# Kernel tuning notes

Measured on AMD Instinct MI355X. Metric: run time of the kernel, lower is better.

Reference implementation:

```python
import jax, jax.numpy as jnp
import numpy as np

DIM = 48
D_STATE = 16
D_CONV = 4
EXPAND = 2
D_INNER = DIM * EXPAND          # 96
DT_RANK = (DIM + 15) // 16      # 3
EPS = 1e-5


def _interp2x_align_corners(x, axis):
    """Linear 2x upsample along one axis with align_corners=True."""
    n = x.shape[axis]
    out = 2 * n
    pos = jnp.arange(out, dtype=jnp.float32) * (n - 1) / (out - 1)
    lo = jnp.floor(pos).astype(jnp.int32)
    hi = jnp.minimum(lo + 1, n - 1)
    w = (pos - lo.astype(jnp.float32)).astype(x.dtype)
    shape = [1] * x.ndim
    shape[axis] = out
    w = w.reshape(shape)
    return jnp.take(x, lo, axis=axis) * (1 - w) + jnp.take(x, hi, axis=axis) * w


def _upsample_trilinear2x(x):
    for axis in (2, 3, 4):
        x = _interp2x_align_corners(x, axis)
    return x


def _conv3d(x, w, b, pad):
    y = jax.lax.conv_general_dilated(
        x, w, window_strides=(1, 1, 1), padding=[(pad, pad)] * 3,
        dimension_numbers=('NCDHW', 'OIDHW', 'NCDHW'))
    return y + b[None, :, None, None, None]


def _instance_norm(x):
    m = x.mean(axis=(2, 3, 4), keepdims=True)
    v = x.var(axis=(2, 3, 4), keepdims=True)  # biased var, as PyTorch InstanceNorm3d
    return (x - m) / jnp.sqrt(v + EPS)


def _mamba(u, in_proj_w, conv1d_w, conv1d_b, x_proj_w, dt_proj_w, dt_proj_b,
           A_log, D_param, out_proj_w):
    # u: (B, L, d_model)
    Bsz, L, _ = u.shape
    xz = jnp.einsum('bld,ed->ble', u, in_proj_w)        # (B, L, 2*Di)
    xi, z = jnp.split(xz, 2, axis=-1)                   # each (B, L, Di)
    # depthwise causal conv1d (pad left d_conv-1, crop to L == mamba's slice)
    xpad = jnp.pad(xi.transpose(0, 2, 1), ((0, 0), (0, 0), (D_CONV - 1, 0)))
    xc = jax.lax.conv_general_dilated(
        xpad, conv1d_w, window_strides=(1,), padding=[(0, 0)],
        dimension_numbers=('NCH', 'OIH', 'NCH'), feature_group_count=D_INNER)
    xs = jax.nn.silu((xc + conv1d_b[None, :, None]).transpose(0, 2, 1))  # (B, L, Di)

    dbc = jnp.einsum('bld,ed->ble', xs, x_proj_w)       # (B, L, dt_rank+2*N)
    dt, Bm, Cm = jnp.split(dbc, [DT_RANK, DT_RANK + D_STATE], axis=-1)
    delta = jax.nn.softplus(jnp.einsum('blr,dr->bld', dt, dt_proj_w) + dt_proj_b)

    A = -jnp.exp(A_log)                                  # (Di, N)
    dA = jnp.exp(jnp.einsum('bld,dn->bldn', delta, A))   # (B, L, Di, N)
    dBx = jnp.einsum('bld,bln->bldn', delta * xs, Bm)    # (B, L, Di, N)

    def step(h, inp):
        dA_t, dBx_t, C_t = inp                           # (B,Di,N),(B,Di,N),(B,N)
        h = dA_t * h + dBx_t
        y = jnp.einsum('bdn,bn->bd', h, C_t)
        return h, y

    h0 = jnp.zeros((Bsz, D_INNER, D_STATE), xs.dtype)
    _, ys = jax.lax.scan(step, h0,
                         (dA.transpose(1, 0, 2, 3), dBx.transpose(1, 0, 2, 3),
                          Cm.transpose(1, 0, 2)))
    y = ys.transpose(1, 0, 2) + D_param[None, None, :] * xs
    y = y * jax.nn.silu(z)
    return jnp.einsum('bld,ed->ble', y, out_proj_w)      # (B, L, d_model)


def setup_inputs() -> dict:
    key = jax.random.key(0)
    ks = jax.random.split(key, 16)
    s = 0.05
    f32 = jnp.float32
    inp = {
        'x': jax.random.normal(ks[0], (2, DIM, 12, 12, 12), f32),
        'Hx': jax.random.normal(ks[1], (2, DIM * 2, 24, 24, 24), f32),
        'W1': jax.random.normal(ks[2], (DIM, DIM * 3, 1, 1, 1), f32) * s,
        'b1': jax.random.normal(ks[3], (DIM,), f32) * s,
        'W2': jax.random.normal(ks[4], (DIM, DIM, 3, 3, 3), f32) * s,
        'b2': jax.random.normal(ks[5], (DIM,), f32) * s,
        'W3': jax.random.normal(ks[6], (DIM, DIM, 1, 1, 1), f32) * s,
        'b3': jax.random.normal(ks[7], (DIM,), f32) * s,
        'in_proj_w': jax.random.normal(ks[8], (2 * D_INNER, DIM), f32) * s,
        'conv1d_w': jax.random.normal(ks[9], (D_INNER, 1, D_CONV), f32) * s,
        'conv1d_b': jax.random.normal(ks[10], (D_INNER,), f32) * s,
        'x_proj_w': jax.random.normal(ks[11], (DT_RANK + 2 * D_STATE, D_INNER), f32) * s,
        'dt_proj_w': jax.random.normal(ks[12], (D_INNER, DT_RANK), f32) * s,
        'dt_proj_b': jax.random.normal(ks[13], (D_INNER,), f32) * 0.1,
        'A_log': jnp.log(jnp.tile(jnp.arange(1, D_STATE + 1, dtype=f32)[None, :],
                                  (D_INNER, 1))),
        'D_param': jnp.ones((D_INNER,), f32),
        'out_proj_w': jax.random.normal(ks[14], (DIM, D_INNER), f32) * s,
    }
    return inp


def reference(x, Hx, W1, b1, W2, b2, W3, b3, in_proj_w, conv1d_w, conv1d_b,
              x_proj_w, dt_proj_w, dt_proj_b, A_log, D_param, out_proj_w):
    up = _upsample_trilinear2x(x)                         # (B, dim, 2H, 2W, 2T)
    h = jnp.concatenate([up, Hx], axis=1)                 # (B, 3*dim, ...)
    h = _conv3d(h, W1, b1, 0)
    h = _conv3d(h, W2, b2, 1)
    h = _conv3d(h, W3, b3, 0)
    Lx = jax.nn.selu(_instance_norm(h))
    B, C, H, W, T = Lx.shape
    u = Lx.reshape(B, C, H * W * T).transpose(0, 2, 1)    # (B, L, C)
    ym = _mamba(u, in_proj_w, conv1d_w, conv1d_b, x_proj_w, dt_proj_w,
                dt_proj_b, A_log, D_param, out_proj_w)
    out = ym.transpose(0, 2, 1).reshape(B, C, H, W, T) + Lx
    return out
```

## Files before the change

### kernel.cpp

```cpp
#include <hip/hip_runtime.h>
#include <math.h>

#define NB 2
#define NCH 48
#define P 13824
#define DI 96
#define NSTATE 16
#define L 13824
#define CHUNK 128
#define NCK 108
#define TL 64

__device__ __forceinline__ float siluf(float x) { return x / (1.f + __expf(-x)); }
__device__ __forceinline__ float softplusf(float x) {
    return x > 0.f ? x + log1pf(expf(-x)) : log1pf(expf(x));
}

__global__ __launch_bounds__(256) void k_wtrans(const float* __restrict__ W2,
    const float* __restrict__ W1, const float* __restrict__ W3,
    const float* __restrict__ Wop, float* __restrict__ Wt, float* __restrict__ W1t,
    float* __restrict__ W3t, float* __restrict__ Wopt)
{
    int i = blockIdx.x * 256 + threadIdx.x;
    if (i < 62208) {
        int o = i / (48 * 27); int r = i % (48 * 27); int c = r / 27; int tap = r % 27;
        int og = o / 12, oi = o % 12;
        Wt[(((og * 48 + c) * 27 + tap) * 12) + oi] = W2[i];
    } else if (i < 62208 + 6912) {
        int j = i - 62208; int o = j / 144, c = j % 144;
        W1t[c * 48 + o] = W1[j];
    } else if (i < 62208 + 6912 + 2304) {
        int j = i - 62208 - 6912; int o = j / 48, c = j % 48;
        W3t[c * 48 + o] = W3[j];
    } else if (i < 62208 + 6912 + 2304 + 4608) {
        int j = i - 62208 - 6912 - 2304; int o = j / 96, q = j % 96;
        Wopt[q * 48 + o] = Wop[j];
    }
}

__global__ __launch_bounds__(128) void k_conv1(const float* __restrict__ x,
    const float* __restrict__ Hx, const float* __restrict__ W1t,
    const float* __restrict__ b1, float* __restrict__ h1)
{
    int t = blockIdx.x * 128 + threadIdx.x;
    int oh = blockIdx.y * 24;
    int b = t / P, p = t % P;
    int zi = p / 576, yi = (p / 24) % 24, xi_ = p % 24;
    float fpos; int z0, z1, y0, y1, x0, x1; float wz, wy, wx;
    fpos = (float)(zi * 11) / 23.0f; z0 = (int)floorf(fpos); wz = fpos - z0; z1 = min(z0 + 1, 11);
    fpos = (float)(yi * 11) / 23.0f; y0 = (int)floorf(fpos); wy = fpos - y0; y1 = min(y0 + 1, 11);
    fpos = (float)(xi_ * 11) / 23.0f; x0 = (int)floorf(fpos); wx = fpos - x0; x1 = min(x0 + 1, 11);
    int o000 = (z0*12+y0)*12+x0, o001 = (z0*12+y0)*12+x1;
    int o010 = (z0*12+y1)*12+x0, o011 = (z0*12+y1)*12+x1;
    int o100 = (z1*12+y0)*12+x0, o101 = (z1*12+y0)*12+x1;
    int o110 = (z1*12+y1)*12+x0, o111 = (z1*12+y1)*12+x1;
    float uz = 1.f - wz, uy = 1.f - wy, ux = 1.f - wx;
    float w000 = uz*uy*ux, w001 = uz*uy*wx, w010 = uz*wy*ux, w011 = uz*wy*wx;
    float w100 = wz*uy*ux, w101 = wz*uy*wx, w110 = wz*wy*ux, w111 = wz*wy*wx;

    float acc[24];
#pragma unroll
    for (int o = 0; o < 24; ++o) acc[o] = b1[oh + o];
    const float* xb = x + (size_t)b * 48 * 1728;
    for (int c0 = 0; c0 < 48; c0 += 4) {
        float a[4][8];
#pragma unroll
        for (int j = 0; j < 4; ++j) {
            const float* xc = xb + (c0 + j) * 1728;
            a[j][0] = xc[o000]; a[j][1] = xc[o001]; a[j][2] = xc[o010]; a[j][3] = xc[o011];
            a[j][4] = xc[o100]; a[j][5] = xc[o101]; a[j][6] = xc[o110]; a[j][7] = xc[o111];
        }
#pragma unroll
        for (int j = 0; j < 4; ++j) {
            float v = a[j][0]*w000 + a[j][1]*w001 + a[j][2]*w010 + a[j][3]*w011
                    + a[j][4]*w100 + a[j][5]*w101 + a[j][6]*w110 + a[j][7]*w111;
            const float* wr = W1t + (c0 + j) * 48 + oh;
#pragma unroll
            for (int o = 0; o < 24; ++o) acc[o] = fmaf(wr[o], v, acc[o]);
        }
    }
    const float* hb = Hx + (size_t)b * 96 * P + p;
    for (int c0 = 0; c0 < 96; c0 += 8) {
        float v[8];
#pragma unroll
        for (int j = 0; j < 8; ++j) v[j] = hb[(size_t)(c0 + j) * P];
#pragma unroll
        for (int j = 0; j < 8; ++j) {
            const float* wr = W1t + (48 + c0 + j) * 48 + oh;
#pragma unroll
            for (int o = 0; o < 24; ++o) acc[o] = fmaf(wr[o], v[j], acc[o]);
        }
    }
    float* out = h1 + (size_t)b * 48 * P + p;
#pragma unroll
    for (int o = 0; o < 24; ++o) out[(size_t)(oh+o) * P] = acc[o];
}

__global__ __launch_bounds__(512) void k_conv2(const float* __restrict__ h1,
    const float* __restrict__ Wt, const float* __restrict__ b2, float* __restrict__ h2)
{
    __shared__ float tile[48 * 240];
    int blk = blockIdx.x;
    int b = blk / 216; int r = blk % 216;
    int tz = r / 36, ty = (r / 6) % 6, tx = r % 6;
    int z0 = tz*4 - 1, y0 = ty*4 - 1, x0 = tx*4 - 1;
    for (int i = threadIdx.x; i < 48 * 216; i += 512) {
        int c = i / 216; int q = i % 216;
        int lz = q / 36, ly = (q / 6) % 6, lx = q % 6;
        int gz = z0 + lz, gy = y0 + ly, gx = x0 + lx;
        float v = 0.f;
        if ((unsigned)gz < 24u && (unsigned)gy < 24u && (unsigned)gx < 24u)
            v = h1[((size_t)(b*48 + c)) * P + (gz*24 + gy)*24 + gx];
        tile[c*240 + lz*40 + ly*6 + lx] = v;
    }
    __syncthreads();
    int lp = threadIdx.x & 63;
    int w  = __builtin_amdgcn_readfirstlane((int)(threadIdx.x >> 6));
    int og = w & 3, cc = w >> 2;
    int lz = lp >> 4, ly = (lp >> 2) & 3, lx = lp & 3;
    float acc[12];
#pragma unroll
    for (int i = 0; i < 12; ++i) acc[i] = cc ? 0.f : b2[og*12 + i];
    const float* wb = Wt + ((size_t)og * 48 + cc * 24) * 27 * 12;
    const float* tb = tile + cc * 24 * 240;
    for (int cl = 0; cl < 24; ++cl) {
        const float* tc = tb + cl * 240;
        const float* wc = wb + cl * 27 * 12;
#pragma unroll
        for (int dz = 0; dz < 3; ++dz)
#pragma unroll
        for (int dy = 0; dy < 3; ++dy)
#pragma unroll
        for (int dx = 0; dx < 3; ++dx) {
            float v = tc[(lz+dz)*40 + (ly+dy)*6 + (lx+dx)];
            const float* wt = wc + ((dz*3 + dy)*3 + dx) * 12;
#pragma unroll
            for (int i = 0; i < 12; ++i)
                acc[i] = fmaf(wt[i], v, acc[i]);
        }
    }
    __syncthreads();
    if (cc == 1) {
        float* ex = tile + og * 768;
#pragma unroll
        for (int i = 0; i < 12; ++i) ex[i*64 + lp] = acc[i];
    }
    __syncthreads();
    if (cc == 0) {
        const float* ex = tile + og * 768;
        int gz = tz*4 + lz, gy = ty*4 + ly, gx = tx*4 + lx;
        size_t pp = (size_t)(gz*24 + gy)*24 + gx;
#pragma unroll
        for (int i = 0; i < 12; ++i)
            h2[((size_t)(b*48) + og*12 + i) * P + pp] = acc[i] + ex[i*64 + lp];
    }
}

__global__ __launch_bounds__(128) void k_conv3(const float* __restrict__ h2,
    const float* __restrict__ W3t, const float* __restrict__ b3, float* __restrict__ h3)
{
    int t = blockIdx.x * 128 + threadIdx.x;
    int oh = blockIdx.y * 24;
    int b = t / P, p = t % P;
    float acc[24];
#pragma unroll
    for (int o = 0; o < 24; ++o) acc[o] = b3[oh + o];
    const float* hb = h2 + (size_t)b * 48 * P + p;
    for (int c0 = 0; c0 < 48; c0 += 8) {
        float v[8];
#pragma unroll
        for (int j = 0; j < 8; ++j) v[j] = hb[(size_t)(c0 + j) * P];
#pragma unroll
        for (int j = 0; j < 8; ++j) {
            const float* wr = W3t + (c0 + j) * 48 + oh;
#pragma unroll
            for (int o = 0; o < 24; ++o) acc[o] = fmaf(wr[o], v[j], acc[o]);
        }
    }
    float* out = h3 + (size_t)b * 48 * P + p;
#pragma unroll
    for (int o = 0; o < 24; ++o) out[(size_t)(oh+o) * P] = acc[o];
}

__global__ __launch_bounds__(256) void k_in_stats(const float* __restrict__ h3,
                                                  float* __restrict__ stats)
{
    int bc = blockIdx.x;
    const float4* src4 = (const float4*)(h3 + (size_t)bc * P);
    float s = 0.f, s2 = 0.f;
    for (int i = threadIdx.x; i < 3456; i += 256) {
        float4 v = src4[i];
        s  += v.x + v.y + v.z + v.w;
        s2 += v.x*v.x + v.y*v.y + v.z*v.z + v.w*v.w;
    }
    __shared__ float rs[4], rs2[4];
    for (int off = 32; off; off >>= 1) { s += __shfl_down(s, off); s2 += __shfl_down(s2, off); }
    int wid = threadIdx.x >> 6;
    if ((threadIdx.x & 63) == 0) { rs[wid] = s; rs2[wid] = s2; }
    __syncthreads();
    if (threadIdx.x == 0) {
        s = rs[0] + rs[1] + rs[2] + rs[3];
        s2 = rs2[0] + rs2[1] + rs2[2] + rs2[3];
        float m = s / (float)P;
        float var = s2 / (float)P - m * m;
        stats[bc*2] = m;
        stats[bc*2 + 1] = rsqrtf(var + 1e-5f);
    }
}

__global__ __launch_bounds__(256) void k_in_apply(float* __restrict__ h3,
                                                  const float* __restrict__ stats)
{
    int t = blockIdx.x * 256 + threadIdx.x;
    int bc = t / P;
    float m = stats[bc*2], istd = stats[bc*2 + 1];
    float v = (h3[t] - m) * istd;
    const float kScale = 1.0507009873554805f, kAlpha = 1.6732632423543772f;
    h3[t] = v > 0.f ? kScale * v : kScale * kAlpha * expm1f(v);
}

__global__ __launch_bounds__(192) void k_inproj(const float* __restrict__ Lx,
    const float* __restrict__ Wip, float* __restrict__ xi, float* __restrict__ z)
{
    __shared__ float u[48 * 32];
    int b = blockIdx.x / 432; int l0 = (blockIdx.x % 432) * 32;
    for (int i = threadIdx.x; i < 48 * 32; i += 192) {
        int c = i >> 5, ll = i & 31;
        u[i] = Lx[((size_t)(b*48) + c) * P + l0 + ll];
    }
    __syncthreads();
    int e = threadIdx.x;
    float w[48];
#pragma unroll
    for (int c = 0; c < 48; ++c) w[c] = Wip[e*48 + c];
    float* dst = (e < 96) ? (xi + ((size_t)b * L + l0) * 96 + e)
                          : (z  + ((size_t)b * L + l0) * 96 + (e - 96));
    for (int ll = 0; ll < 32; ++ll) {
        float acc = 0.f;
#pragma unroll
        for (int c = 0; c < 48; ++c) acc = fmaf(w[c], u[c*32 + ll], acc);
        dst[(size_t)ll * 96] = acc;
    }
}

__global__ __launch_bounds__(256) void k_fxproj(const float* __restrict__ xi,
    const float* __restrict__ cw, const float* __restrict__ cb,
    const float* __restrict__ Wxp, const float* __restrict__ Wdt,
    const float* __restrict__ bdt, float* __restrict__ xs,
    float* __restrict__ delta, float* __restrict__ Bm, float* __restrict__ Cm)
{
    __shared__ float xs_t[TL][100];
    __shared__ float wx_t[35][100];
    __shared__ float wd_t[96][4];
    __shared__ float dt_t[TL][4];
    int blk = blockIdx.x;
    int b = blk / 216; int l0 = (blk % 216) * TL;
    int tid = threadIdx.x;

    for (int i = tid; i < 35 * 96; i += 256) wx_t[i / 96][i % 96] = Wxp[i];
    for (int i = tid; i < 96 * 3; i += 256) wd_t[i / 3][i % 3] = Wdt[i];
    for (int i = tid; i < 96; i += 256) wd_t[i][3] = bdt[i];

    int row = tid >> 2;
    int d0 = (tid & 3) * 24;
    int l = l0 + row;
    size_t t_glob = (size_t)b * L + l;
    const float* xib = xi + (size_t)b * L * 96;
    float* xsg = xs + t_glob * 96 + d0;
    int ls0 = l - 3;
#pragma unroll
    for (int jq = 0; jq < 6; ++jq) {
        int d = d0 + jq * 4;
        float4 t0 = *(const float4*)(cw + 4 * (d + 0));
        float4 t1 = *(const float4*)(cw + 4 * (d + 1));
        float4 t2 = *(const float4*)(cw + 4 * (d + 2));
        float4 t3 = *(const float4*)(cw + 4 * (d + 3));
        float4 acc = *(const float4*)(cb + d);
        float4 q0 = {0.f,0.f,0.f,0.f}, q1 = q0, q2 = q0;
        if (ls0 + 0 >= 0) q0 = *(const float4*)(xib + (size_t)(ls0 + 0) * 96 + d);
        if (ls0 + 1 >= 0) q1 = *(const float4*)(xib + (size_t)(ls0 + 1) * 96 + d);
        if (ls0 + 2 >= 0) q2 = *(const float4*)(xib + (size_t)(ls0 + 2) * 96 + d);
        float4 q3 = *(const float4*)(xib + (size_t)(ls0 + 3) * 96 + d);
        acc.x += t0.x*q0.x + t0.y*q1.x + t0.z*q2.x + t0.w*q3.x;
        acc.y += t1.x*q0.y + t1.y*q1.y + t1.z*q2.y + t1.w*q3.y;
        acc.z += t2.x*q0.z + t2.y*q1.z + t2.z*q2.z + t2.w*q3.z;
        acc.w += t3.x*q0.w + t3.y*q1.w + t3.z*q2.w + t3.w*q3.w;
        acc.x = siluf(acc.x); acc.y = siluf(acc.y);
        acc.z = siluf(acc.z); acc.w = siluf(acc.w);
        *(float4*)(&xs_t[row][d0 + jq * 4]) = acc;
        *(float4*)(xsg + jq * 4) = acc;
    }
    __syncthreads();

    int cq = tid & 3;
    float acc9[9];
#pragma unroll
    for (int k = 0; k < 9; ++k) acc9[k] = 0.f;
    const float* xrow = &xs_t[row][0];
#pragma unroll 4
    for (int j = 0; j < 24; ++j) {
        float4 xv = *(const float4*)(xrow + 4 * j);
#pragma unroll
        for (int k = 0; k < 9; ++k) {
            if (k < 8 || cq < 3) {
                int e = cq + 4 * k;
                float4 wv = *(const float4*)(&wx_t[e][4 * j]);
                acc9[k] = fmaf(wv.x, xv.x, fmaf(wv.y, xv.y,
                          fmaf(wv.z, xv.z, fmaf(wv.w, xv.w, acc9[k]))));
            }
        }
    }
#pragma unroll
    for (int k = 0; k < 9; ++k) {
        if (k < 8 || cq < 3) {
            int e = cq + 4 * k;
            if (e < 3)       dt_t[row][e] = acc9[k];
            else if (e < 19) Bm[t_glob * 16 + (e - 3)]  = acc9[k];
            else             Cm[t_glob * 16 + (e - 19)] = acc9[k];
        }
    }
    __syncthreads();

    float dt0 = dt_t[row][0], dt1 = dt_t[row][1], dt2 = dt_t[row][2];
    float* dl = delta + t_glob * 96 + d0;
#pragma unroll
    for (int jq = 0; jq < 6; ++jq) {
        float4 o;
        {
            float4 wv = *(const float4*)(&wd_t[d0 + jq*4 + 0][0]);
            o.x = softplusf(fmaf(wv.x, dt0, fmaf(wv.y, dt1, fmaf(wv.z, dt2, wv.w))));
        }
        {
            float4 wv = *(const float4*)(&wd_t[d0 + jq*4 + 1][0]);
            o.y = softplusf(fmaf(wv.x, dt0, fmaf(wv.y, dt1, fmaf(wv.z, dt2, wv.w))));
        }
        {
            float4 wv = *(const float4*)(&wd_t[d0 + jq*4 + 2][0]);
            o.z = softplusf(fmaf(wv.x, dt0, fmaf(wv.y, dt1, fmaf(wv.z, dt2, wv.w))));
        }
        {
            float4 wv = *(const float4*)(&wd_t[d0 + jq*4 + 3][0]);
            o.w = softplusf(fmaf(wv.x, dt0, fmaf(wv.y, dt1, fmaf(wv.z, dt2, wv.w))));
        }
        *(float4*)(dl + jq * 4) = o;
    }
}

__global__ __launch_bounds__(256) void k_scan1(const float* __restrict__ delta,
    const float* __restrict__ xs, const float* __restrict__ Bm,
    const float* __restrict__ Alog, float* __restrict__ Aprod, float* __restrict__ hend)
{
    int wid = (blockIdx.x * 256 + threadIdx.x) >> 6;
    int lane = threadIdx.x & 63;
    int dg = wid % 24; int ch = (wid / 24) % NCK; int b = wid / (24 * NCK);
    int dl = lane >> 4, n = lane & 15;
    int d = dg * 4 + dl;
    float A = -__expf(Alog[d*16 + n]);
    float h = 0.f, ap = 1.f;
    int t0 = ch * CHUNK;
    const float* dp = delta + ((size_t)b * L + t0) * 96 + d;
    const float* xp = xs    + ((size_t)b * L + t0) * 96 + d;
    const float* bp = Bm    + ((size_t)b * L + t0) * 16 + n;

    float dA0, dA1, dA2, dA3, xA0, xA1, xA2, xA3, bA0, bA1, bA2, bA3;
    float dB0, dB1, dB2, dB3, xB0, xB1, xB2, xB3, bB0, bB1, bB2, bB3;
#define LD1(s, T) do { \
    d##s##0 = dp[(size_t)(T)*96];     x##s##0 = xp[(size_t)(T)*96];     b##s##0 = bp[(size_t)(T)*16]; \
    d##s##1 = dp[(size_t)((T)+1)*96]; x##s##1 = xp[(size_t)((T)+1)*96]; b##s##1 = bp[(size_t)((T)+1)*16]; \
    d##s##2 = dp[(size_t)((T)+2)*96]; x##s##2 = xp[(size_t)((T)+2)*96]; b##s##2 = bp[(size_t)((T)+2)*16]; \
    d##s##3 = dp[(size_t)((T)+3)*96]; x##s##3 = xp[(size_t)((T)+3)*96]; b##s##3 = bp[(size_t)((T)+3)*16]; \
  } while (0)
#define CMP1(s) do { \
    float e0 = __expf(d##s##0 * A); float e1 = __expf(d##s##1 * A); \
    float e2 = __expf(d##s##2 * A); float e3 = __expf(d##s##3 * A); \
    h = fmaf(e0, h, d##s##0 * x##s##0 * b##s##0); \
    h = fmaf(e1, h, d##s##1 * x##s##1 * b##s##1); \
    h = fmaf(e2, h, d##s##2 * x##s##2 * b##s##2); \
    h = fmaf(e3, h, d##s##3 * x##s##3 * b##s##3); \
    ap *= e0 * e1 * e2 * e3; \
  } while (0)

    LD1(A, 0);
#pragma unroll 1
    for (int t = 0; t < CHUNK; t += 8) {
        LD1(B, t + 4);
        CMP1(A);
        if (t + 8 < CHUNK) LD1(A, t + 8);
        CMP1(B);
    }
#undef LD1
#undef CMP1
    size_t idx = (((size_t)b * NCK + ch) * 96 + d) * 16 + n;
    Aprod[idx] = ap;
    hend[idx]  = h;
}

__global__ __launch_bounds__(256) void k_scan2(const float* __restrict__ Aprod,
    const float* __restrict__ hend, float* __restrict__ hin)
{
    int t = blockIdx.x * 256 + threadIdx.x;
    int b = t / 1536; int dn = t % 1536;
    const float* ap = Aprod + (size_t)b * NCK * 1536 + dn;
    const float* he = hend  + (size_t)b * NCK * 1536 + dn;
    float* hi       = hin   + (size_t)b * NCK * 1536 + dn;
    float carry = 0.f;
    float aA0, aA1, aA2, aA3, hA0, hA1, hA2, hA3;
    float aB0, aB1, aB2, aB3, hB0, hB1, hB2, hB3;
#define LD2(s, J) do { \
    a##s##0 = ap[(size_t)(J)*1536];     h##s##0 = he[(size_t)(J)*1536]; \
    a##s##1 = ap[(size_t)((J)+1)*1536]; h##s##1 = he[(size_t)((J)+1)*1536]; \
    a##s##2 = ap[(size_t)((J)+2)*1536]; h##s##2 = he[(size_t)((J)+2)*1536]; \
    a##s##3 = ap[(size_t)((J)+3)*1536]; h##s##3 = he[(size_t)((J)+3)*1536]; \
  } while (0)
#define CMP2(s, J) do { \
    hi[(size_t)(J)*1536]     = carry; carry = fmaf(a##s##0, carry, h##s##0); \
    hi[(size_t)((J)+1)*1536] = carry; carry = fmaf(a##s##1, carry, h##s##1); \
    hi[(size_t)((J)+2)*1536] = carry; carry = fmaf(a##s##2, carry, h##s##2); \
    hi[(size_t)((J)+3)*1536] = carry; carry = fmaf(a##s##3, carry, h##s##3); \
  } while (0)
    LD2(A, 0);
#pragma unroll 1
    for (int j = 0; j < 104; j += 8) {
        LD2(B, j + 4);
        CMP2(A, j);
        if (j + 8 < NCK) LD2(A, j + 8);
        CMP2(B, j + 4);
    }
    LD2(A, 104);
    CMP2(A, 104);
#undef LD2
#undef CMP2
}

__global__ __launch_bounds__(256) void k_scan3(const float* __restrict__ delta,
    float* __restrict__ xs, const float* __restrict__ Bm, const float* __restrict__ Cm,
    const float* __restrict__ z, const float* __restrict__ Alog,
    const float* __restrict__ Dp, const float* __restrict__ hin)
{
    int wid = (blockIdx.x * 256 + threadIdx.x) >> 6;
    int lane = threadIdx.x & 63;
    int dg = wid % 24; int ch = (wid / 24) % NCK; int b = wid / (24 * NCK);
    int dl = lane >> 4, n = lane & 15;
    int d = dg * 4 + dl;
    float A = -__expf(Alog[d*16 + n]);
    float Dv = Dp[d];
    size_t cidx = (((size_t)b * NCK + ch) * 96 + d) * 16 + n;
    float h = hin[cidx];
    int t0 = ch * CHUNK;
    const float* dp = delta + ((size_t)b * L + t0) * 96 + d;
    float* xp       = xs    + ((size_t)b * L + t0) * 96 + d;
    const float* bp = Bm    + ((size_t)b * L + t0) * 16 + n;
    const float* cp = Cm    + ((size_t)b * L + t0) * 16 + n;
    const float* zp = z     + ((size_t)b * L + t0) * 96 + d;

    float dA0, dA1, dA2, dA3, xA0, xA1, xA2, xA3, bA0, bA1, bA2, bA3, cA0, cA1, cA2, cA3, zA0, zA1, zA2, zA3;
    float dB0, dB1, dB2, dB3, xB0, xB1, xB2, xB3, bB0, bB1, bB2, bB3, cB0, cB1, cB2, cB3, zB0, zB1, zB2, zB3;
#define LD3(s, T) do { \
    d##s##0 = dp[(size_t)(T)*96];     x##s##0 = xp[(size_t)(T)*96];     b##s##0 = bp[(size_t)(T)*16]; \
    c##s##0 = cp[(size_t)(T)*16];     z##s##0 = zp[(size_t)(T)*96]; \
    d##s##1 = dp[(size_t)((T)+1)*96]; x##s##1 = xp[(size_t)((T)+1)*96]; b##s##1 = bp[(size_t)((T)+1)*16]; \
    c##s##1 = cp[(size_t)((T)+1)*16]; z##s##1 = zp[(size_t)((T)+1)*96]; \
    d##s##2 = dp[(size_t)((T)+2)*96]; x##s##2 = xp[(size_t)((T)+2)*96]; b##s##2 = bp[(size_t)((T)+2)*16]; \
    c##s##2 = cp[(size_t)((T)+2)*16]; z##s##2 = zp[(size_t)((T)+2)*96]; \
    d##s##3 = dp[(size_t)((T)+3)*96]; x##s##3 = xp[(size_t)((T)+3)*96]; b##s##3 = bp[(size_t)((T)+3)*16]; \
    c##s##3 = cp[(size_t)((T)+3)*16]; z##s##3 = zp[(size_t)((T)+3)*96]; \
  } while (0)
#define STEP3(DEL, XV, BV, CV, ZV, T) do { \
    float dAv = __expf((DEL) * A); \
    h = fmaf(dAv, h, (DEL) * (XV) * (BV)); \
    float yc = h * (CV); \
    yc += __shfl_xor(yc, 8); \
    yc += __shfl_xor(yc, 4); \
    yc += __shfl_xor(yc, 2); \
    yc += __shfl_xor(yc, 1); \
    if (n == 0) xp[(size_t)(T)*96] = fmaf(Dv, (XV), yc) * siluf(ZV); \
  } while (0)
#define CMP3(s, T) do { \
    STEP3(d##s##0, x##s##0, b##s##0, c##s##0, z##s##0, (T)); \
    STEP3(d##s##1, x##s##1, b##s##1, c##s##1, z##s##1, (T)+1); \
    STEP3(d##s##2, x##s##2, b##s##2, c##s##2, z##s##2, (T)+2); \
    STEP3(d##s##3, x##s##3, b##s##3, c##s##3, z##s##3, (T)+3); \
  } while (0)

    LD3(A, 0);
#pragma unroll 1
    for (int t = 0; t < CHUNK; t += 8) {
        LD3(B, t + 4);
        CMP3(A, t);
        if (t + 8 < CHUNK) LD3(A, t + 8);
        CMP3(B, t + 4);
    }
#undef LD3
#undef STEP3
#undef CMP3
}

__global__ __launch_bounds__(128) void k_outproj(const float* __restrict__ y,
    const float* __restrict__ Wopt, const float* __restrict__ Lx, float* __restrict__ out)
{
    int t = blockIdx.x * 128 + threadIdx.x;
    int oh = blockIdx.y * 24;
    int b = t / P, p = t % P;
    const float* yr = y + (size_t)t * 96;
    float acc[24];
#pragma unroll
    for (int o = 0; o < 24; ++o) acc[o] = 0.f;
#pragma unroll
    for (int i = 0; i < 24; ++i) {
        float4 v4 = ((const float4*)yr)[i];
        const float* w0 = Wopt + (i*4) * 48 + oh;
        const float* w1 = Wopt + (i*4 + 1) * 48 + oh;
        const float* w2 = Wopt + (i*4 + 2) * 48 + oh;
        const float* w3 = Wopt + (i*4 + 3) * 48 + oh;
#pragma unroll
        for (int o = 0; o < 24; ++o) {
            acc[o] = fmaf(w0[o], v4.x, acc[o]);
            acc[o] = fmaf(w1[o], v4.y, acc[o]);
            acc[o] = fmaf(w2[o], v4.z, acc[o]);
            acc[o] = fmaf(w3[o], v4.w, acc[o]);
        }
    }
    const float* lx = Lx + (size_t)b * 48 * P + p;
    float* op = out + (size_t)b * 48 * P + p;
#pragma unroll
    for (int o = 0; o < 24; ++o) op[(size_t)(oh+o) * P] = acc[o] + lx[(size_t)(oh+o) * P];
}

extern "C" void kernel_launch(void* const* d_in, const int* in_sizes, int n_in,
                              void* d_out, int out_size, void* d_ws, size_t ws_size,
                              hipStream_t stream) {
    const float* x        = (const float*)d_in[0];
    const float* Hx       = (const float*)d_in[1];
    const float* W1       = (const float*)d_in[2];
    const float* b1       = (const float*)d_in[3];
    const float* W2       = (const float*)d_in[4];
    const float* b2       = (const float*)d_in[5];
    const float* W3       = (const float*)d_in[6];
    const float* b3       = (const float*)d_in[7];
    const float* in_proj  = (const float*)d_in[8];
    const float* conv1d_w = (const float*)d_in[9];
    const float* conv1d_b = (const float*)d_in[10];
    const float* x_proj   = (const float*)d_in[11];
    const float* dt_proj  = (const float*)d_in[12];
    const float* dt_bias  = (const float*)d_in[13];
    const float* A_log    = (const float*)d_in[14];
    const float* D_param  = (const float*)d_in[15];
    const float* out_proj = (const float*)d_in[16];
    float* out = (float*)d_out;

    float* ws = (float*)d_ws;
    const size_t SZ_BCP = (size_t)NB * 48 * P;
    const size_t SZ_BLD = (size_t)NB * L * 96;
    const size_t SZ_BLN = (size_t)NB * L * 16;
    const size_t SZ_CK  = (size_t)NB * NCK * 1536;
    float* bufA  = ws;
    float* bufB  = bufA + SZ_BCP;
    float* bufC  = bufB + SZ_BCP;
    float* xib   = bufC + SZ_BCP;
    float* zb    = xib  + SZ_BLD;
    float* xsb   = zb   + SZ_BLD;
    float* Bmb   = xsb  + SZ_BLD;
    float* Cmb   = Bmb  + SZ_BLN;
    float* Apr   = Cmb  + SZ_BLN;
    float* hendb = Apr  + SZ_CK;
    float* hinb  = hendb+ SZ_CK;
    float* stats = hinb + SZ_CK;
    float* Wtb   = stats + 192;
    float* W1tb  = Wtb + 62208;
    float* W3tb  = W1tb + 6912;
    float* Woptb = W3tb + 2304;
    float* deltab = bufA;

    k_wtrans<<<297, 256, 0, stream>>>(W2, W1, W3, out_proj, Wtb, W1tb, W3tb, Woptb);
    k_conv1<<<dim3(216, 2), 128, 0, stream>>>(x, Hx, W1tb, b1, bufA);
    k_conv2<<<NB * 216, 512, 0, stream>>>(bufA, Wtb, b2, bufB);
    k_conv3<<<dim3(216, 2), 128, 0, stream>>>(bufB, W3tb, b3, bufC);
    k_in_stats<<<NB * 48, 256, 0, stream>>>(bufC, stats);
    k_in_apply<<<5184, 256, 0, stream>>>(bufC, stats);
    k_inproj<<<NB * 432, 192, 0, stream>>>(bufC, in_proj, xib, zb);
    k_fxproj<<<NB * 216, 256, 0, stream>>>(xib, conv1d_w, conv1d_b, x_proj, dt_proj,
                                           dt_bias, xsb, deltab, Bmb, Cmb);
    k_scan1<<<(NB * NCK * 24) / 4, 256, 0, stream>>>(deltab, xsb, Bmb, A_log, Apr, hendb);
    k_scan2<<<12, 256, 0, stream>>>(Apr, hendb, hinb);
    k_scan3<<<(NB * NCK * 24) / 4, 256, 0, stream>>>(deltab, xsb, Bmb, Cmb, zb, A_log,
                                                     D_param, hinb);
    k_outproj<<<dim3(216, 2), 128, 0, stream>>>(xsb, Woptb, bufC, out);
}
```

Measured before the change: 286.8 us.

## Fuse conv2 with 1x1 conv3, merge instance-norm passes, drop inproj LDS staging

The 1x1x1 conv3 now runs inside the conv2 kernel. Conv2 results are staged in shared memory and each wave computes 6 output channels, so the h2 round trip through global memory and one launch are gone. Instance-norm statistics and the normalize+SELU apply become a single kernel per channel that rereads its slice, which removes a launch and the stats buffer. In-proj now reads Lx directly from global memory with register accumulators instead of staging it in LDS. The trade-offs are serialized per-channel work in the norm kernel (only 96 blocks) and higher register pressure in in-proj.

```diff
diff --git a/kernel.cpp b/kernel.cpp
--- a/kernel.cpp
+++ b/kernel.cpp
@@ -96,8 +96,10 @@
     for (int o = 0; o < 24; ++o) out[(size_t)(oh+o) * P] = acc[o];
 }
 
-__global__ __launch_bounds__(512) void k_conv2(const float* __restrict__ h1,
-    const float* __restrict__ Wt, const float* __restrict__ b2, float* __restrict__ h2)
+__global__ __launch_bounds__(512) void k_conv23(const float* __restrict__ h1,
+    const float* __restrict__ Wt, const float* __restrict__ b2,
+    const float* __restrict__ W3t, const float* __restrict__ b3,
+    float* __restrict__ h3)
 {
     __shared__ float tile[48 * 240];
     int blk = blockIdx.x;
@@ -148,52 +150,41 @@
     __syncthreads();
     if (cc == 0) {
         const float* ex = tile + og * 768;
-        int gz = tz*4 + lz, gy = ty*4 + ly, gx = tx*4 + lx;
-        size_t pp = (size_t)(gz*24 + gy)*24 + gx;
+        float* ht = tile + 3072;
 #pragma unroll
         for (int i = 0; i < 12; ++i)
-            h2[((size_t)(b*48) + og*12 + i) * P + pp] = acc[i] + ex[i*64 + lp];
-    }
-}
-
-__global__ __launch_bounds__(128) void k_conv3(const float* __restrict__ h2,
-    const float* __restrict__ W3t, const float* __restrict__ b3, float* __restrict__ h3)
-{
-    int t = blockIdx.x * 128 + threadIdx.x;
-    int oh = blockIdx.y * 24;
-    int b = t / P, p = t % P;
-    float acc[24];
-#pragma unroll
-    for (int o = 0; o < 24; ++o) acc[o] = b3[oh + o];
-    const float* hb = h2 + (size_t)b * 48 * P + p;
-    for (int c0 = 0; c0 < 48; c0 += 8) {
-        float v[8];
-#pragma unroll
-        for (int j = 0; j < 8; ++j) v[j] = hb[(size_t)(c0 + j) * P];
-#pragma unroll
-        for (int j = 0; j < 8; ++j) {
-            const float* wr = W3t + (c0 + j) * 48 + oh;
-#pragma unroll
-            for (int o = 0; o < 24; ++o) acc[o] = fmaf(wr[o], v[j], acc[o]);
-        }
-    }
-    float* out = h3 + (size_t)b * 48 * P + p;
-#pragma unroll
-    for (int o = 0; o < 24; ++o) out[(size_t)(oh+o) * P] = acc[o];
-}
-
-__global__ __launch_bounds__(256) void k_in_stats(const float* __restrict__ h3,
-                                                  float* __restrict__ stats)
+            ht[(og*12 + i)*64 + lp] = acc[i] + ex[i*64 + lp];
+    }
+    __syncthreads();
+    const float* ht = tile + 3072;
+    int oc0 = w * 6;
+    float acc3[6];
+#pragma unroll
+    for (int j = 0; j < 6; ++j) acc3[j] = b3[oc0 + j];
+    for (int c = 0; c < 48; ++c) {
+        float v = ht[c*64 + lp];
+        const float* wr = W3t + c*48 + oc0;
+#pragma unroll
+        for (int j = 0; j < 6; ++j) acc3[j] = fmaf(wr[j], v, acc3[j]);
+    }
+    int gz = tz*4 + lz, gy = ty*4 + ly, gx = tx*4 + lx;
+    size_t pp = (size_t)(gz*24 + gy)*24 + gx;
+#pragma unroll
+    for (int j = 0; j < 6; ++j)
+        h3[((size_t)(b*48) + oc0 + j) * P + pp] = acc3[j];
+}
+
+__global__ __launch_bounds__(256) void k_instnorm(float* __restrict__ h3)
 {
     int bc = blockIdx.x;
-    const float4* src4 = (const float4*)(h3 + (size_t)bc * P);
+    float4* src = (float4*)(h3 + (size_t)bc * P);
     float s = 0.f, s2 = 0.f;
     for (int i = threadIdx.x; i < 3456; i += 256) {
-        float4 v = src4[i];
+        float4 v = src[i];
         s  += v.x + v.y + v.z + v.w;
         s2 += v.x*v.x + v.y*v.y + v.z*v.z + v.w*v.w;
     }
-    __shared__ float rs[4], rs2[4];
+    __shared__ float rs[4], rs2[4], mv[2];
     for (int off = 32; off; off >>= 1) { s += __shfl_down(s, off); s2 += __shfl_down(s2, off); }
     int wid = threadIdx.x >> 6;
     if ((threadIdx.x & 63) == 0) { rs[wid] = s; rs2[wid] = s2; }
@@ -203,44 +194,45 @@
         s2 = rs2[0] + rs2[1] + rs2[2] + rs2[3];
         float m = s / (float)P;
         float var = s2 / (float)P - m * m;
-        stats[bc*2] = m;
-        stats[bc*2 + 1] = rsqrtf(var + 1e-5f);
-    }
-}
-
-__global__ __launch_bounds__(256) void k_in_apply(float* __restrict__ h3,
-                                                  const float* __restrict__ stats)
-{
-    int t = blockIdx.x * 256 + threadIdx.x;
-    int bc = t / P;
-    float m = stats[bc*2], istd = stats[bc*2 + 1];
-    float v = (h3[t] - m) * istd;
-    const float kScale = 1.0507009873554805f, kAlpha = 1.6732632423543772f;
-    h3[t] = v > 0.f ? kScale * v : kScale * kAlpha * expm1f(v);
+        mv[0] = m; mv[1] = rsqrtf(var + 1e-5f);
+    }
+    __syncthreads();
+    float m = mv[0], istd = mv[1];
+    const float kS = 1.0507009873554805f, kA = 1.6732632423543772f;
+    for (int i = threadIdx.x; i < 3456; i += 256) {
+        float4 v = src[i];
+        float a0 = (v.x - m) * istd, a1 = (v.y - m) * istd;
+        float a2 = (v.z - m) * istd, a3 = (v.w - m) * istd;
+        v.x = a0 > 0.f ? kS * a0 : kS * kA * expm1f(a0);
+        v.y = a1 > 0.f ? kS * a1 : kS * kA * expm1f(a1);
+        v.z = a2 > 0.f ? kS * a2 : kS * kA * expm1f(a2);
+        v.w = a3 > 0.f ? kS * a3 : kS * kA * expm1f(a3);
+        src[i] = v;
+    }
 }
 
 __global__ __launch_bounds__(192) void k_inproj(const float* __restrict__ Lx,
     const float* __restrict__ Wip, float* __restrict__ xi, float* __restrict__ z)
 {
-    __shared__ float u[48 * 32];
     int b = blockIdx.x / 432; int l0 = (blockIdx.x % 432) * 32;
-    for (int i = threadIdx.x; i < 48 * 32; i += 192) {
-        int c = i >> 5, ll = i & 31;
-        u[i] = Lx[((size_t)(b*48) + c) * P + l0 + ll];
-    }
-    __syncthreads();
     int e = threadIdx.x;
     float w[48];
 #pragma unroll
     for (int c = 0; c < 48; ++c) w[c] = Wip[e*48 + c];
+    float acc[32];
+#pragma unroll
+    for (int ll = 0; ll < 32; ++ll) acc[ll] = 0.f;
+    const float* ub = Lx + (size_t)b * 48 * P + l0;
+#pragma unroll 2
+    for (int c = 0; c < 48; ++c) {
+        const float* ur = ub + (size_t)c * P;
+#pragma unroll
+        for (int ll = 0; ll < 32; ++ll) acc[ll] = fmaf(w[c], ur[ll], acc[ll]);
+    }
     float* dst = (e < 96) ? (xi + ((size_t)b * L + l0) * 96 + e)
                           : (z  + ((size_t)b * L + l0) * 96 + (e - 96));
-    for (int ll = 0; ll < 32; ++ll) {
-        float acc = 0.f;
-#pragma unroll
-        for (int c = 0; c < 48; ++c) acc = fmaf(w[c], u[c*32 + ll], acc);
-        dst[(size_t)ll * 96] = acc;
-    }
+#pragma unroll
+    for (int ll = 0; ll < 32; ++ll) dst[(size_t)ll * 96] = acc[ll];
 }
 
 __global__ __launch_bounds__(256) void k_fxproj(const float* __restrict__ xi,
@@ -573,10 +565,8 @@
 
     k_wtrans<<<297, 256, 0, stream>>>(W2, W1, W3, out_proj, Wtb, W1tb, W3tb, Woptb);
     k_conv1<<<dim3(216, 2), 128, 0, stream>>>(x, Hx, W1tb, b1, bufA);
-    k_conv2<<<NB * 216, 512, 0, stream>>>(bufA, Wtb, b2, bufB);
-    k_conv3<<<dim3(216, 2), 128, 0, stream>>>(bufB, W3tb, b3, bufC);
-    k_in_stats<<<NB * 48, 256, 0, stream>>>(bufC, stats);
-    k_in_apply<<<5184, 256, 0, stream>>>(bufC, stats);
+    k_conv23<<<NB * 216, 512, 0, stream>>>(bufA, Wtb, b2, W3tb, b3, bufC);
+    k_instnorm<<<NB * 48, 256, 0, stream>>>(bufC);
     k_inproj<<<NB * 432, 192, 0, stream>>>(bufC, in_proj, xib, zb);
     k_fxproj<<<NB * 216, 256, 0, stream>>>(xib, conv1d_w, conv1d_b, x_proj, dt_proj,
                                            dt_bias, xsb, deltab, Bmb, Cmb);
```

Result: faster. 275.0 us (-4.1%).
